# Kernel optimization log

Measured on AMD Instinct MI355X. Metric: run time of the kernel, lower is better.

The kernel has to match this reference:

```python
import jax, jax.numpy as jnp
import numpy as np

D_MODEL = 1024
NUM_HEADS = 16
HEAD_DIM = D_MODEL // NUM_HEADS


def setup_inputs() -> dict:
    key = jax.random.key(0)
    kq, kk, kv, k1, k2, k3, k4 = jax.random.split(key, 7)
    B, S = 4, 2048
    scale = 1.0 / np.sqrt(D_MODEL)
    return {
        "q": jax.random.normal(kq, (B, S, D_MODEL), jnp.float32),
        "k": jax.random.normal(kk, (B, S, D_MODEL), jnp.float32),
        "v": jax.random.normal(kv, (B, S, D_MODEL), jnp.float32),
        "mask": jnp.tril(jnp.ones((S, S), jnp.bool_))[None, None, :, :],  # causal [1,1,S,S]
        "W_q": jax.random.normal(k1, (D_MODEL, D_MODEL), jnp.float32) * scale,
        "W_k": jax.random.normal(k2, (D_MODEL, D_MODEL), jnp.float32) * scale,
        "W_v": jax.random.normal(k3, (D_MODEL, D_MODEL), jnp.float32) * scale,
        "W_o": jax.random.normal(k4, (D_MODEL, D_MODEL), jnp.float32) * scale,
    }


def reference(q, k, v, mask, W_q, W_k, W_v, W_o):
    B, S, _ = q.shape
    H, Dh = NUM_HEADS, HEAD_DIM
    # nn.Linear(x) = x @ W.T ; split heads -> [B, H, S, Dh]
    def proj(x, W):
        return (x @ W.T).reshape(B, -1, H, Dh).transpose(0, 2, 1, 3)
    Q, K, V = proj(q, W_q), proj(k, W_k), proj(v, W_v)
    scores = jnp.einsum("bhqd,bhkd->bhqk", Q, K) / np.sqrt(Dh)
    scores = jnp.where(mask, scores, -1e9)
    attn = jax.nn.softmax(scores, axis=-1)  # dropout_p=0 (eval)
    out = jnp.einsum("bhqk,bhkd->bhqd", attn, V)
    out = out.transpose(0, 2, 1, 3).reshape(B, S, D_MODEL)
    return out @ W_o.T
```

## Files before the change

kernel.cpp:

```cpp
#include <hip/hip_runtime.h>
#include <hip/hip_bf16.h>

typedef __attribute__((ext_vector_type(4))) float  f32x4;
typedef __attribute__((ext_vector_type(8))) short  s16x8;
typedef __attribute__((ext_vector_type(4))) short  s16x4;
typedef unsigned short u16;

constexpr int B_  = 4;
constexpr int S_  = 2048;
constexpr int D_  = 1024;
constexpr int H_  = 16;
constexpr int Dh_ = 64;

#define QSCALE 0.18033688f

static __device__ __forceinline__ short fb(float f) {
    __hip_bfloat16 h = __float2bfloat16(f);
    return __builtin_bit_cast(short, h);
}

static __device__ __forceinline__ void gload16(const void* g, void* l) {
    __builtin_amdgcn_global_load_lds(
        (const __attribute__((address_space(1))) unsigned int*)g,
        (__attribute__((address_space(3))) unsigned int*)l, 16, 0, 0);
}

__global__ __launch_bounds__(256)
void cvtW(const float* __restrict__ s0, const float* __restrict__ s1,
          const float* __restrict__ s2, const float* __restrict__ s3,
          u16* __restrict__ d0, u16* __restrict__ d1,
          u16* __restrict__ d2, u16* __restrict__ d3)
{
    const int y = blockIdx.y;
    const float* s = y == 0 ? s0 : (y == 1 ? s1 : (y == 2 ? s2 : s3));
    u16*         d = y == 0 ? d0 : (y == 1 ? d1 : (y == 2 ? d2 : d3));
    long i = ((long)blockIdx.x * 256 + threadIdx.x) * 8;
    f32x4 a = *(const f32x4*)(s + i), b = *(const f32x4*)(s + i + 4);
    s16x8 o;
    #pragma unroll
    for (int j = 0; j < 4; ++j) { o[j] = fb(a[j]); o[4 + j] = fb(b[j]); }
    *(s16x8*)(d + i) = o;
}

__global__ __launch_bounds__(512)
void gemmQKV(const float* __restrict__ qin, const float* __restrict__ kin,
             const float* __restrict__ vin,
             const u16* __restrict__ WqB, const u16* __restrict__ WkB,
             const u16* __restrict__ WvB,
             u16* __restrict__ Qp, u16* __restrict__ Kt, u16* __restrict__ Vt)
{
    __shared__ u16 As[2][4096];
    __shared__ u16 Bs[2][8192];

    const int z = blockIdx.z;
    const float* A  = z == 0 ? qin : (z == 1 ? kin : vin);
    const u16*   Wb = z == 0 ? WqB : (z == 1 ? WkB : WvB);

    const int m0 = blockIdx.x * 128, n0 = blockIdx.y * 256;
    const int t = threadIdx.x, lane = t & 63, w = t >> 6;
    const int wr = (w >> 2) * 64, wc = (w & 3) * 64;
    const int lr = lane & 15, lg = lane >> 4;

    const int srow = t >> 2;
    const int cc   = (t & 3) ^ ((t >> 3) & 3);
    const int fcol = (lg ^ ((lr >> 1) & 3)) * 8;

    const u16* Brow = Wb + (long)(n0 + srow) * 1024 + cc * 8;
    const float* Af = A + (long)(m0 + srow) * 1024 + (t & 3) * 8;

    f32x4 acc[4][4] = {};

    {
        f32x4 a0 = *(const f32x4*)(Af);
        f32x4 a1 = *(const f32x4*)(Af + 4);
        s16x8 oA;
        #pragma unroll
        for (int j = 0; j < 4; ++j) { oA[j] = fb(a0[j]); oA[4 + j] = fb(a1[j]); }
        *(s16x8*)(&As[0][srow * 32 + cc * 8]) = oA;
    }
    gload16(Brow,              Bs[0] + w * 512);
    gload16(Brow + 128 * 1024, Bs[0] + 4096 + w * 512);
    __syncthreads();

    for (int step = 0; step < 32; ++step) {
        const int cur = step & 1, nxt = cur ^ 1;
        const int k1 = (step + 1) * 32;
        const bool more = step + 1 < 32;

        f32x4 a0, a1;
        if (more) {
            a0 = *(const f32x4*)(Af + k1);
            a1 = *(const f32x4*)(Af + k1 + 4);
            gload16(Brow + k1,              Bs[nxt] + w * 512);
            gload16(Brow + 128 * 1024 + k1, Bs[nxt] + 4096 + w * 512);
        }

        s16x8 af[4], bfr[4];
        #pragma unroll
        for (int i = 0; i < 4; ++i)
            af[i] = *(const s16x8*)(&As[cur][(wr + i * 16 + lr) * 32 + fcol]);
        #pragma unroll
        for (int i = 0; i < 4; ++i)
            bfr[i] = *(const s16x8*)(&Bs[cur][(wc + i * 16 + lr) * 32 + fcol]);
        #pragma unroll
        for (int mi = 0; mi < 4; ++mi)
            #pragma unroll
            for (int ni = 0; ni < 4; ++ni)
                acc[mi][ni] = __builtin_amdgcn_mfma_f32_16x16x32_bf16(
                    af[mi], bfr[ni], acc[mi][ni], 0, 0, 0);

        if (more) {
            s16x8 oA;
            #pragma unroll
            for (int j = 0; j < 4; ++j) { oA[j] = fb(a0[j]); oA[4 + j] = fb(a1[j]); }
            *(s16x8*)(&As[nxt][srow * 32 + cc * 8]) = oA;
        }
        __syncthreads();
    }

    if (z == 0) {
        #pragma unroll
        for (int mi = 0; mi < 4; ++mi)
            #pragma unroll
            for (int ni = 0; ni < 4; ++ni) {
                int col = n0 + wc + ni * 16 + lr;
                int h = col >> 6, dh = col & 63;
                #pragma unroll
                for (int r = 0; r < 4; ++r) {
                    int row = m0 + wr + mi * 16 + lg * 4 + r;
                    int b = row >> 11, s = row & 2047;
                    Qp[(((long)b * H_ + h) * S_ + s) * Dh_ + dh] =
                        (u16)fb(acc[mi][ni][r] * QSCALE);
                }
            }
    } else if (z == 1) {
        #pragma unroll
        for (int mi = 0; mi < 4; ++mi)
            #pragma unroll
            for (int ni = 0; ni < 4; ++ni) {
                int col = n0 + wc + ni * 16 + lr;
                int h = col >> 6, dh = col & 63;
                #pragma unroll
                for (int r = 0; r < 4; ++r) {
                    int row = m0 + wr + mi * 16 + lg * 4 + r;
                    int b = row >> 11, s = row & 2047;
                    long idx = ((long)(b * H_ + h)) * 131072 + ((long)(s >> 6) << 12)
                             + ((s & 63) << 6) + (((dh >> 3) ^ (s & 7)) << 3) + (dh & 7);
                    Kt[idx] = (u16)fb(acc[mi][ni][r]);
                }
            }
    } else {
        #pragma unroll
        for (int mi = 0; mi < 4; ++mi)
            #pragma unroll
            for (int ni = 0; ni < 4; ++ni) {
                int col = n0 + wc + ni * 16 + lr;
                int h = col >> 6, dh = col & 63;
                int row = m0 + wr + mi * 16 + lg * 4;
                int b = row >> 11, k = row & 2047;
                long idx = ((long)(b * H_ + h)) * 131072 + ((long)(k >> 6) << 12)
                         + (dh << 6) + ((((k >> 3) & 7) ^ (dh & 7)) << 3) + (k & 7);
                union { short h4[4]; unsigned long long u; } pk;
                #pragma unroll
                for (int r = 0; r < 4; ++r) pk.h4[r] = fb(acc[mi][ni][r]);
                *(unsigned long long*)(&Vt[idx]) = pk.u;
            }
    }
}

__global__ __launch_bounds__(256)
void gemmO(const u16* __restrict__ Av, const u16* __restrict__ Wb,
           float* __restrict__ C)
{
    __shared__ u16 As[2][4096];
    __shared__ u16 Bs[2][4096];

    const int m0 = blockIdx.x * 128, n0 = blockIdx.y * 128;
    const int t = threadIdx.x, lane = t & 63, w = t >> 6;
    const int wr = (w >> 1) * 64, wc = (w & 1) * 64;
    const int lr = lane & 15, lg = lane >> 4;

    const int srow = t >> 2;
    const int cc   = (t & 3) ^ ((t >> 3) & 3);
    const int fcol = (lg ^ ((lr >> 1) & 3)) * 8;

    const u16* Brow = Wb + (long)(n0 + srow) * 1024 + cc * 8;
    const u16* Arow = Av + (long)(m0 + srow) * 1024 + cc * 8;

    f32x4 acc[4][4] = {};

    gload16(Arow,             As[0] + w * 512);
    gload16(Arow + 64 * 1024, As[0] + 2048 + w * 512);
    gload16(Brow,             Bs[0] + w * 512);
    gload16(Brow + 64 * 1024, Bs[0] + 2048 + w * 512);
    __syncthreads();

    for (int step = 0; step < 32; ++step) {
        const int cur = step & 1, nxt = cur ^ 1;
        const int k1 = (step + 1) * 32;
        if (step + 1 < 32) {
            gload16(Arow + k1,             As[nxt] + w * 512);
            gload16(Arow + 64 * 1024 + k1, As[nxt] + 2048 + w * 512);
            gload16(Brow + k1,             Bs[nxt] + w * 512);
            gload16(Brow + 64 * 1024 + k1, Bs[nxt] + 2048 + w * 512);
        }
        s16x8 af[4], bfr[4];
        #pragma unroll
        for (int i = 0; i < 4; ++i)
            af[i] = *(const s16x8*)(&As[cur][(wr + i * 16 + lr) * 32 + fcol]);
        #pragma unroll
        for (int i = 0; i < 4; ++i)
            bfr[i] = *(const s16x8*)(&Bs[cur][(wc + i * 16 + lr) * 32 + fcol]);
        #pragma unroll
        for (int mi = 0; mi < 4; ++mi)
            #pragma unroll
            for (int ni = 0; ni < 4; ++ni)
                acc[mi][ni] = __builtin_amdgcn_mfma_f32_16x16x32_bf16(
                    af[mi], bfr[ni], acc[mi][ni], 0, 0, 0);
        __syncthreads();
    }

    #pragma unroll
    for (int mi = 0; mi < 4; ++mi)
        #pragma unroll
        for (int ni = 0; ni < 4; ++ni) {
            int col = n0 + wc + ni * 16 + lr;
            #pragma unroll
            for (int r = 0; r < 4; ++r) {
                int row = m0 + wr + mi * 16 + lg * 4 + r;
                C[(long)row * 1024 + col] = acc[mi][ni][r];
            }
        }
}

__global__ __launch_bounds__(256)
void attn(const u16* __restrict__ Qp, const u16* __restrict__ Kws,
          const u16* __restrict__ Vws, u16* __restrict__ Op)
{
    __shared__ u16 Klds[2][4096];
    __shared__ u16 Vlds[2][4096];

    const int t = threadIdx.x, lane = t & 63, w = t >> 6;
    const int lr = lane & 15, lg = lane >> 4;
    const int strip = 15 - (int)(blockIdx.x >> 6);
    const int bh = blockIdx.x & 63;
    const int b = bh >> 4, h = bh & 15;
    const int q0w = strip * 128 + w * 32;

    const u16* Kb = Kws + (long)bh * 131072;
    const u16* Vb = Vws + (long)bh * 131072;
    const u16* Qbp = Qp + ((long)bh * S_ + q0w) * Dh_;

    const int nkb = (strip + 1) * 2;

    s16x8 qf[2][2];
    #pragma unroll
    for (int i = 0; i < 2; ++i)
        #pragma unroll
        for (int hh = 0; hh < 2; ++hh)
            qf[i][hh] = *(const s16x8*)(Qbp + (i * 16 + lr) * Dh_ + hh * 32 + lg * 8);

    auto stage = [&](int kb, int buf) {
        const long go = (long)kb * 4096 + (2 * w) * 512 + lane * 8;
        gload16(Kb + go,       &Klds[buf][(2 * w) * 512]);
        gload16(Kb + go + 512, &Klds[buf][(2 * w + 1) * 512]);
        gload16(Vb + go,       &Vlds[buf][(2 * w) * 512]);
        gload16(Vb + go + 512, &Vlds[buf][(2 * w + 1) * 512]);
    };

    f32x4 acc[2][4] = {};
    float mrun[2] = { -1e30f, -1e30f }, lrun[2] = { 0.0f, 0.0f };

    stage(0, 0);
    __syncthreads();

    #pragma unroll 1
    for (int kb = 0; kb < nkb; ++kb) {
        const int cur = kb & 1;
        const int k0 = kb * 64;
        if (kb + 1 < nkb) stage(kb + 1, cur ^ 1);
        if (k0 <= q0w + 31) {
            f32x4 st[2][4] = {};
            const int r7 = lr & 7;
            __builtin_amdgcn_s_setprio(1);
            #pragma unroll
            for (int kt = 0; kt < 4; ++kt) {
                const int rb = (kt * 16 + lr) * 64;
                s16x8 kf0 = *(const s16x8*)(&Klds[cur][rb + ((lg ^ r7) << 3)]);
                s16x8 kf1 = *(const s16x8*)(&Klds[cur][rb + (((4 + lg) ^ r7) << 3)]);
                #pragma unroll
                for (int i = 0; i < 2; ++i) {
                    st[i][kt] = __builtin_amdgcn_mfma_f32_16x16x32_bf16(
                        kf0, qf[i][0], st[i][kt], 0, 0, 0);
                    st[i][kt] = __builtin_amdgcn_mfma_f32_16x16x32_bf16(
                        kf1, qf[i][1], st[i][kt], 0, 0, 0);
                }
            }
            __builtin_amdgcn_s_setprio(0);

            const bool dmask = (k0 + 63) > q0w;
            s16x4 pb[2][4];
            #pragma unroll
            for (int i = 0; i < 2; ++i) {
                const int qg = q0w + i * 16 + lr;
                float sv[16];
                if (dmask) {
                    #pragma unroll
                    for (int kt = 0; kt < 4; ++kt)
                        #pragma unroll
                        for (int rr = 0; rr < 4; ++rr) {
                            float sc = st[i][kt][rr];
                            if ((k0 + kt * 16 + lg * 4 + rr) > qg) sc = -1e30f;
                            sv[kt * 4 + rr] = sc;
                        }
                } else {
                    #pragma unroll
                    for (int kt = 0; kt < 4; ++kt)
                        #pragma unroll
                        for (int rr = 0; rr < 4; ++rr)
                            sv[kt * 4 + rr] = st[i][kt][rr];
                }
                float t0 = fmaxf(fmaxf(sv[0], sv[1]), sv[2]);
                float t1 = fmaxf(fmaxf(sv[3], sv[4]), sv[5]);
                float t2 = fmaxf(fmaxf(sv[6], sv[7]), sv[8]);
                float t3 = fmaxf(fmaxf(sv[9], sv[10]), sv[11]);
                float t4 = fmaxf(fmaxf(sv[12], sv[13]), sv[14]);
                float tm = fmaxf(fmaxf(fmaxf(t0, t1), t2),
                                 fmaxf(fmaxf(t3, t4), sv[15]));
                tm = fmaxf(tm, __shfl_xor(tm, 16));
                tm = fmaxf(tm, __shfl_xor(tm, 32));
                float mnew = mrun[i];
                if (!__all(tm <= mrun[i] + 8.0f)) {
                    mnew = fmaxf(mrun[i], tm);
                    float f = __builtin_amdgcn_exp2f(mrun[i] - mnew);
                    lrun[i] *= f;
                    #pragma unroll
                    for (int tt = 0; tt < 4; ++tt) acc[i][tt] *= f;
                    mrun[i] = mnew;
                }
                float psum = 0.0f;
                #pragma unroll
                for (int kt = 0; kt < 4; ++kt) {
                    short ph[4];
                    #pragma unroll
                    for (int rr = 0; rr < 4; ++rr) {
                        float p = __builtin_amdgcn_exp2f(sv[kt * 4 + rr] - mnew);
                        psum += p;
                        ph[rr] = fb(p);
                    }
                    pb[i][kt] = (s16x4){ ph[0], ph[1], ph[2], ph[3] };
                }
                lrun[i] += psum;
            }

            __builtin_amdgcn_s_setprio(1);
            #pragma unroll
            for (int kt = 0; kt < 4; ++kt)
                #pragma unroll
                for (int tt = 0; tt < 4; ++tt) {
                    const int rb = (tt * 16 + lr) * 64;
                    const int gsw = (kt * 2 + (lg >> 1)) ^ r7;
                    s16x4 vf = *(const s16x4*)
                        (&Vlds[cur][rb + (gsw << 3) + ((lg & 1) << 2)]);
                    acc[0][tt] = __builtin_amdgcn_mfma_f32_16x16x16bf16_1k(
                        vf, pb[0][kt], acc[0][tt], 0, 0, 0);
                    acc[1][tt] = __builtin_amdgcn_mfma_f32_16x16x16bf16_1k(
                        vf, pb[1][kt], acc[1][tt], 0, 0, 0);
                }
            __builtin_amdgcn_s_setprio(0);
        }
        __syncthreads();
    }

    #pragma unroll
    for (int i = 0; i < 2; ++i) {
        float l = lrun[i];
        l += __shfl_xor(l, 16);
        l += __shfl_xor(l, 32);
        const float inv = 1.0f / l;
        u16* ob = Op + (((long)b * S_ + q0w + i * 16 + lr) * H_ + h) * Dh_;
        #pragma unroll
        for (int tt = 0; tt < 4; ++tt) {
            union { short h4[4]; unsigned long long u; } pk;
            #pragma unroll
            for (int rr = 0; rr < 4; ++rr) pk.h4[rr] = fb(acc[i][tt][rr] * inv);
            *(unsigned long long*)(ob + tt * 16 + lg * 4) = pk.u;
        }
    }
}

extern "C" void kernel_launch(void* const* d_in, const int* in_sizes, int n_in,
                              void* d_out, int out_size, void* d_ws, size_t ws_size,
                              hipStream_t stream)
{
    const float* q  = (const float*)d_in[0];
    const float* k  = (const float*)d_in[1];
    const float* v  = (const float*)d_in[2];
    const float* Wq = (const float*)d_in[4];
    const float* Wk = (const float*)d_in[5];
    const float* Wv = (const float*)d_in[6];
    const float* Wo = (const float*)d_in[7];

    u16* ws = (u16*)d_ws;
    const long NE = (long)B_ * S_ * D_;
    const long WE = (long)D_ * D_;
    u16* Qp  = ws;
    u16* Kws_ = ws + NE;
    u16* Vws_ = ws + 2 * NE;
    u16* Op  = ws + 3 * NE;
    u16* WqB = Op;
    u16* WkB = Op + WE;
    u16* WvB = Op + 2 * WE;

    const bool woExtra = ws_size >= (size_t)(4 * NE + WE) * 2;
    u16* WoB = woExtra ? (ws + 4 * NE) : Qp;

    dim3 blk(256);
    if (woExtra) {
        hipLaunchKernelGGL(cvtW, dim3(512, 4), blk, 0, stream,
                           Wq, Wk, Wv, Wo, WqB, WkB, WvB, WoB);
    } else {
        hipLaunchKernelGGL(cvtW, dim3(512, 3), blk, 0, stream,
                           Wq, Wk, Wv, Wo, WqB, WkB, WvB, WoB);
    }
    hipLaunchKernelGGL(gemmQKV, dim3(64, 4, 3), dim3(512), 0, stream,
                       q, k, v, WqB, WkB, WvB, Qp, Kws_, Vws_);
    hipLaunchKernelGGL(attn, dim3(1024), blk, 0, stream, Qp, Kws_, Vws_, Op);
    if (!woExtra) {
        hipLaunchKernelGGL(cvtW, dim3(512, 1), blk, 0, stream,
                           Wo, Wo, Wo, Wo, WoB, WoB, WoB, WoB);
    }
    hipLaunchKernelGGL(gemmO, dim3(64, 8), blk, 0, stream, Op, WoB, (float*)d_out);
}
```

Before: 187.6 us.

## Retile QKV GEMM to 128x128 with 256 threads and triple-buffered pipeline

Changes the fused QKV projection GEMM from 128x256 tiles with 512 threads to 128x128 tiles with 256 threads, doubling the grid. It adds a three-stage LDS ring with two A-register sets, prefetching two k-steps ahead. Explicit vmcnt/lgkmcnt waits and sched barriers replace __syncthreads. The aim is better overlap of global loads with MFMA work and more blocks per CU, at the cost of more A loads per thread and fragile hand-counted wait values.

```diff
diff --git a/kernel.cpp b/kernel.cpp
--- a/kernel.cpp
+++ b/kernel.cpp
@@ -42,23 +42,23 @@
     *(s16x8*)(d + i) = o;
 }
 
-__global__ __launch_bounds__(512)
+__global__ __launch_bounds__(256)
 void gemmQKV(const float* __restrict__ qin, const float* __restrict__ kin,
              const float* __restrict__ vin,
              const u16* __restrict__ WqB, const u16* __restrict__ WkB,
              const u16* __restrict__ WvB,
              u16* __restrict__ Qp, u16* __restrict__ Kt, u16* __restrict__ Vt)
 {
-    __shared__ u16 As[2][4096];
-    __shared__ u16 Bs[2][8192];
+    __shared__ u16 As[3][4096];
+    __shared__ u16 Bs[3][4096];
 
     const int z = blockIdx.z;
     const float* A  = z == 0 ? qin : (z == 1 ? kin : vin);
     const u16*   Wb = z == 0 ? WqB : (z == 1 ? WkB : WvB);
 
-    const int m0 = blockIdx.x * 128, n0 = blockIdx.y * 256;
+    const int m0 = blockIdx.x * 128, n0 = blockIdx.y * 128;
     const int t = threadIdx.x, lane = t & 63, w = t >> 6;
-    const int wr = (w >> 2) * 64, wc = (w & 3) * 64;
+    const int wr = (w >> 1) * 64, wc = (w & 1) * 64;
     const int lr = lane & 15, lg = lane >> 4;
 
     const int srow = t >> 2;
@@ -69,53 +69,78 @@
     const float* Af = A + (long)(m0 + srow) * 1024 + (t & 3) * 8;
 
     f32x4 acc[4][4] = {};
-
-    {
-        f32x4 a0 = *(const f32x4*)(Af);
-        f32x4 a1 = *(const f32x4*)(Af + 4);
-        s16x8 oA;
-        #pragma unroll
-        for (int j = 0; j < 4; ++j) { oA[j] = fb(a0[j]); oA[4 + j] = fb(a1[j]); }
-        *(s16x8*)(&As[0][srow * 32 + cc * 8]) = oA;
-    }
-    gload16(Brow,              Bs[0] + w * 512);
-    gload16(Brow + 128 * 1024, Bs[0] + 4096 + w * 512);
-    __syncthreads();
-
-    for (int step = 0; step < 32; ++step) {
-        const int cur = step & 1, nxt = cur ^ 1;
-        const int k1 = (step + 1) * 32;
-        const bool more = step + 1 < 32;
-
-        f32x4 a0, a1;
-        if (more) {
-            a0 = *(const f32x4*)(Af + k1);
-            a1 = *(const f32x4*)(Af + k1 + 4);
-            gload16(Brow + k1,              Bs[nxt] + w * 512);
-            gload16(Brow + 128 * 1024 + k1, Bs[nxt] + 4096 + w * 512);
-        }
-
+    f32x4 rE[4], rO[4];
+
+    auto loadA = [&](f32x4 (&r)[4], int k) {
+        r[0] = *(const f32x4*)(Af + k);
+        r[1] = *(const f32x4*)(Af + k + 4);
+        r[2] = *(const f32x4*)(Af + 64 * 1024 + k);
+        r[3] = *(const f32x4*)(Af + 64 * 1024 + k + 4);
+    };
+    auto loadB = [&](int k, int buf) {
+        gload16(Brow + k,             Bs[buf] + w * 512);
+        gload16(Brow + 64 * 1024 + k, Bs[buf] + 2048 + w * 512);
+    };
+    auto cvtA = [&](f32x4 (&r)[4], int buf) {
+        s16x8 oA, oB;
+        #pragma unroll
+        for (int j = 0; j < 4; ++j) {
+            oA[j] = fb(r[0][j]); oA[4 + j] = fb(r[1][j]);
+            oB[j] = fb(r[2][j]); oB[4 + j] = fb(r[3][j]);
+        }
+        *(s16x8*)(&As[buf][srow * 32 + cc * 8])        = oA;
+        *(s16x8*)(&As[buf][(64 + srow) * 32 + cc * 8]) = oB;
+    };
+    auto compute = [&](int buf) {
         s16x8 af[4], bfr[4];
         #pragma unroll
         for (int i = 0; i < 4; ++i)
-            af[i] = *(const s16x8*)(&As[cur][(wr + i * 16 + lr) * 32 + fcol]);
+            af[i] = *(const s16x8*)(&As[buf][(wr + i * 16 + lr) * 32 + fcol]);
         #pragma unroll
         for (int i = 0; i < 4; ++i)
-            bfr[i] = *(const s16x8*)(&Bs[cur][(wc + i * 16 + lr) * 32 + fcol]);
+            bfr[i] = *(const s16x8*)(&Bs[buf][(wc + i * 16 + lr) * 32 + fcol]);
         #pragma unroll
         for (int mi = 0; mi < 4; ++mi)
             #pragma unroll
             for (int ni = 0; ni < 4; ++ni)
                 acc[mi][ni] = __builtin_amdgcn_mfma_f32_16x16x32_bf16(
                     af[mi], bfr[ni], acc[mi][ni], 0, 0, 0);
-
-        if (more) {
-            s16x8 oA;
-            #pragma unroll
-            for (int j = 0; j < 4; ++j) { oA[j] = fb(a0[j]); oA[4 + j] = fb(a1[j]); }
-            *(s16x8*)(&As[nxt][srow * 32 + cc * 8]) = oA;
-        }
-        __syncthreads();
+    };
+
+    loadA(rE, 0);
+    loadA(rO, 32);
+    loadB(0, 0);
+    loadB(32, 1);
+    cvtA(rE, 0);
+    asm volatile("s_waitcnt lgkmcnt(0)" ::: "memory");
+    __builtin_amdgcn_sched_barrier(0);
+    __builtin_amdgcn_s_barrier();
+
+    int c0 = 0, c1 = 1, c2 = 2;
+    #pragma unroll 2
+    for (int step = 0; step < 32; ++step) {
+        if (step + 2 < 32) {
+            if (!(step & 1)) loadA(rE, (step + 2) * 32);
+            else             loadA(rO, (step + 2) * 32);
+            loadB((step + 2) * 32, c2);
+            asm volatile("s_waitcnt vmcnt(8)" ::: "memory");
+        } else if (step == 30) {
+            asm volatile("s_waitcnt vmcnt(6)" ::: "memory");
+        } else {
+            asm volatile("s_waitcnt vmcnt(0)" ::: "memory");
+        }
+        __builtin_amdgcn_sched_barrier(0);
+
+        compute(c0);
+
+        if (step + 1 < 32) {
+            if (!(step & 1)) cvtA(rO, c1);
+            else             cvtA(rE, c1);
+        }
+        asm volatile("s_waitcnt lgkmcnt(0)" ::: "memory");
+        __builtin_amdgcn_sched_barrier(0);
+        __builtin_amdgcn_s_barrier();
+        int tmp = c0; c0 = c1; c1 = c2; c2 = tmp;
     }
 
     if (z == 0) {
@@ -423,7 +448,7 @@
         hipLaunchKernelGGL(cvtW, dim3(512, 3), blk, 0, stream,
                            Wq, Wk, Wv, Wo, WqB, WkB, WvB, WoB);
     }
-    hipLaunchKernelGGL(gemmQKV, dim3(64, 4, 3), dim3(512), 0, stream,
+    hipLaunchKernelGGL(gemmQKV, dim3(64, 8, 3), blk, 0, stream,
                        q, k, v, WqB, WkB, WvB, Qp, Kws_, Vws_);
     hipLaunchKernelGGL(attn, dim3(1024), blk, 0, stream, Qp, Kws_, Vws_, Op);
     if (!woExtra) {
```

Result: slower. 201.4 us (+7.4%).
